# Performance work log

Measured on AMD Instinct MI355X. Metric: run time of the kernel, lower is better.

Reference implementation:

```python
import jax, jax.numpy as jnp
import numpy as np

N, E, G = 100000, 1600000, 5000
F_IN, H = 128, 3
C1, C2, C3 = 64, 32, 16
SLOPE = 0.2


def _gat_conv(x, W, a_src, a_dst, b, src, dst, n_nodes, heads, ch):
    # x: [N, F_in] -> h: [N, H, C]
    h = (x @ W).reshape(n_nodes, heads, ch)
    alpha_s = jnp.sum(h * a_src, axis=-1)  # [N, H]
    alpha_d = jnp.sum(h * a_dst, axis=-1)  # [N, H]
    e = jax.nn.leaky_relu(alpha_s[src] + alpha_d[dst], SLOPE)  # [E, H]
    # segment softmax over destination nodes (numerically stable)
    e_max = jax.ops.segment_max(e, dst, num_segments=n_nodes)
    e_max = jnp.where(jnp.isfinite(e_max), e_max, 0.0)
    ex = jnp.exp(e - e_max[dst])
    denom = jax.ops.segment_sum(ex, dst, num_segments=n_nodes)
    alpha = ex / (denom[dst] + 1e-16)  # [E, H]
    msg = h[src] * alpha[:, :, None]  # [E, H, C]
    out = jax.ops.segment_sum(msg, dst, num_segments=n_nodes)  # [N, H, C]
    return out.reshape(n_nodes, heads * ch) + b


def setup_inputs() -> dict:
    key = jax.random.key(0)
    ks = jax.random.split(key, 20)
    def w(k, shape, fan_in):
        return jax.random.normal(k, shape, jnp.float32) / np.sqrt(fan_in)
    return {
        "x": jax.random.normal(ks[0], (N, F_IN), jnp.float32),
        "y": jax.random.uniform(ks[1], (G,), jnp.float32),
        "edge_index": jax.random.randint(ks[2], (2, E), 0, N, jnp.int32),
        "batch": jnp.sort(jax.random.randint(ks[3], (N,), 0, G, jnp.int32)),
        "W1": w(ks[4], (F_IN, H * C1), F_IN),
        "as1": w(ks[5], (H, C1), C1),
        "ad1": w(ks[6], (H, C1), C1),
        "b1": jnp.zeros((H * C1,), jnp.float32),
        "W2": w(ks[7], (H * C1, H * C2), H * C1),
        "as2": w(ks[8], (H, C2), C2),
        "ad2": w(ks[9], (H, C2), C2),
        "b2": jnp.zeros((H * C2,), jnp.float32),
        "W3": w(ks[10], (H * C2, H * C3), H * C2),
        "as3": w(ks[11], (H, C3), C3),
        "ad3": w(ks[12], (H, C3), C3),
        "b3": jnp.zeros((H * C3,), jnp.float32),
        "Wl": w(ks[13], (H * C3, 1), H * C3),
        "bl": jnp.zeros((1,), jnp.float32),
    }


def reference(x, y, edge_index, batch, W1, as1, ad1, b1, W2, as2, ad2, b2,
              W3, as3, ad3, b3, Wl, bl):
    n = x.shape[0]
    loops = jnp.arange(n, dtype=edge_index.dtype)
    src = jnp.concatenate([edge_index[0], loops])  # PyG add_self_loops=True
    dst = jnp.concatenate([edge_index[1], loops])

    h = _gat_conv(x, W1, as1, ad1, b1, src, dst, n, H, C1)
    h = jax.nn.elu(h)
    h = _gat_conv(h, W2, as2, ad2, b2, src, dst, n, H, C2)
    h = jax.nn.elu(h)
    h = _gat_conv(h, W3, as3, ad3, b3, src, dst, n, H, C3)

    # global mean pool over graphs
    counts = jax.ops.segment_sum(jnp.ones((n,), h.dtype), batch, num_segments=G)
    pooled = jax.ops.segment_sum(h, batch, num_segments=G) / jnp.maximum(counts, 1.0)[:, None]
    pooled = jax.nn.relu(pooled)

    logits = pooled @ Wl + bl  # [G, 1]
    t = y.reshape(-1, 1)
    loss = jnp.mean(jax.nn.softplus(logits) - t * logits)  # BCEWithLogits
    out = jax.nn.sigmoid(logits)
    return out, loss
```

## Files before the change

### kernel.cpp

```cpp
#include <hip/hip_runtime.h>
#include <hip/hip_bf16.h>

#define THREADS 256
typedef __hip_bfloat16 bf16;

typedef __bf16 v8bf __attribute__((ext_vector_type(8)));
typedef float  v4f  __attribute__((ext_vector_type(4)));

__device__ __forceinline__ float bfl(unsigned u){ return __uint_as_float(u << 16); }
__device__ __forceinline__ float bfh(unsigned u){ return __uint_as_float(u & 0xffff0000u); }

__global__ void hist_k(const int* __restrict__ ei, int* __restrict__ cnt,
                       int* __restrict__ rank, int E, int ET){
  int i = blockIdx.x*THREADS + threadIdx.x;
  if (i >= ET) return;
  int d = (i < E) ? ei[E + i] : (i - E);
  rank[i] = atomicAdd(&cnt[d], 1);
}

__global__ void scan1_k(const int* __restrict__ deg, int* __restrict__ off,
                        int* __restrict__ bsum, int n){
  __shared__ int sh[1024];
  int i = blockIdx.x*1024 + threadIdx.x;
  int v = (i < n) ? deg[i] : 0;
  sh[threadIdx.x] = v;
  __syncthreads();
  for (int s = 1; s < 1024; s <<= 1){
    int t = (threadIdx.x >= s) ? sh[threadIdx.x - s] : 0;
    __syncthreads();
    sh[threadIdx.x] += t;
    __syncthreads();
  }
  if (i < n) off[i+1] = sh[threadIdx.x];
  if (threadIdx.x == 1023) bsum[blockIdx.x] = sh[1023];
}

__global__ void scan2_k(int* __restrict__ bsum, int nb){
  __shared__ int sh[256];
  int v = (threadIdx.x < nb) ? bsum[threadIdx.x] : 0;
  sh[threadIdx.x] = v;
  __syncthreads();
  for (int s = 1; s < 256; s <<= 1){
    int t = (threadIdx.x >= s) ? sh[threadIdx.x - s] : 0;
    __syncthreads();
    sh[threadIdx.x] += t;
    __syncthreads();
  }
  if (threadIdx.x < nb) bsum[threadIdx.x] = sh[threadIdx.x] - v;
}

__global__ void scan3_k(int* __restrict__ off, const int* __restrict__ bsum, int n){
  int i = blockIdx.x*1024 + threadIdx.x;
  if (i < n) off[i+1] += bsum[blockIdx.x];
  if (i == 0) off[0] = 0;
}

__global__ void scatter_k(const int* __restrict__ ei, const int* __restrict__ off,
                          const int* __restrict__ rank, int* __restrict__ csr,
                          int E, int ET){
  int i = blockIdx.x*THREADS + threadIdx.x;
  if (i >= ET) return;
  int s, d;
  if (i < E){ s = ei[i]; d = ei[E+i]; } else { s = i - E; d = i - E; }
  csr[off[d] + rank[i]] = s;
}

__global__ void convf2b_k(const float4* __restrict__ in, uint2* __restrict__ out, int n4){
  int i = blockIdx.x*THREADS + threadIdx.x;
  if (i >= n4) return;
  float4 v = in[i];
  union { bf16 h[4]; uint2 u; } cv;
  cv.h[0] = __float2bfloat16(v.x); cv.h[1] = __float2bfloat16(v.y);
  cv.h[2] = __float2bfloat16(v.z); cv.h[3] = __float2bfloat16(v.w);
  out[i] = cv.u;
}

__device__ __forceinline__ void wt_do(const float* __restrict__ W, bf16* __restrict__ WT,
                                      int K, int COUT, int i){
  int k = i / COUT, c = i - k*COUT;
  WT[(size_t)c*K + k] = __float2bfloat16(W[i]);
}

__device__ __forceinline__ void va_do(const float* __restrict__ W, const float* __restrict__ as,
                                      const float* __restrict__ ad, bf16* __restrict__ WTX,
                                      int K, int C, int COUT, int i){
  int k = i % K, c6 = i / K;
  int h = (c6 < 3) ? c6 : c6 - 3;
  const float* a = ((c6 < 3) ? as : ad) + h*C;
  const float* wp = W + (size_t)k*COUT + h*C;
  float s = 0.f;
  for (int cc = 0; cc < C; cc++) s += wp[cc]*a[cc];
  WTX[(size_t)(COUT + c6)*K + k] = __float2bfloat16(s);
}

__global__ void prep_k(const float* __restrict__ W1, const float* __restrict__ as1, const float* __restrict__ ad1,
                       const float* __restrict__ W2, const float* __restrict__ as2, const float* __restrict__ ad2,
                       const float* __restrict__ W3, const float* __restrict__ as3, const float* __restrict__ ad3,
                       bf16* __restrict__ WT1, bf16* __restrict__ WT2, bf16* __restrict__ WT3,
                       const int* __restrict__ batch, int* __restrict__ goff, int n, int G)
{
  int i = blockIdx.x*THREADS + threadIdx.x;
  if (i < 24576){ wt_do(W1, WT1, 128, 192, i); return; } i -= 24576;
  if (i < 18432){ wt_do(W2, WT2, 192, 96, i); return; }  i -= 18432;
  if (i < 4608) { wt_do(W3, WT3, 96, 48, i); return; }   i -= 4608;
  if (i < 768)  { va_do(W1, as1, ad1, WT1, 128, 64, 192, i); return; } i -= 768;
  if (i < 1152) { va_do(W2, as2, ad2, WT2, 192, 32, 96, i); return; }  i -= 1152;
  if (i < 576)  { va_do(W3, as3, ad3, WT3, 96, 16, 48, i); return; }   i -= 576;
  if (i <= G){
    if (i == G){ goff[G] = n; return; }
    int lo = 0, hi = n;
    while (lo < hi){ int mid = (lo + hi) >> 1; if (batch[mid] < i) lo = mid + 1; else hi = mid; }
    goff[i] = lo;
  }
}

template<int K, int COUT>
__global__ void __launch_bounds__(256) gemm_mfma_k(
    const bf16* __restrict__ A, const bf16* __restrict__ BT,
    bf16* __restrict__ C, float* __restrict__ aS4, float* __restrict__ aD4,
    int nRowTiles)
{
  int wave = threadIdx.x >> 6, lane = threadIdx.x & 63;
  int rt = blockIdx.x*4 + wave;
  if (rt >= nRowTiles) return;
  int half = lane & 15;
  int quad = lane >> 4;
  const __bf16* aBase = (const __bf16*)A + (size_t)(rt*16 + half)*K + quad*8;
  v8bf aF[K/32];
  #pragma unroll
  for (int kk = 0; kk < K/32; kk++) aF[kk] = *(const v8bf*)(aBase + kk*32);
  #pragma unroll
  for (int cb = 0; cb < COUT + 16; cb += 16){
    const __bf16* bBase = (const __bf16*)BT + (size_t)(cb + half)*K + quad*8;
    v4f acc = {0.f, 0.f, 0.f, 0.f};
    #pragma unroll
    for (int kk = 0; kk < K/32; kk++)
      acc = __builtin_amdgcn_mfma_f32_16x16x32_bf16(aF[kk], *(const v8bf*)(bBase + kk*32), acc, 0, 0, 0);
    int orow = rt*16 + quad*4;
    if (cb < COUT){
      bf16* cp = C + (size_t)orow*COUT + cb + half;
      #pragma unroll
      for (int r = 0; r < 4; r++)
        cp[(size_t)r*COUT] = __float2bfloat16(acc[r]);
    } else if (half < 6){
      #pragma unroll
      for (int r = 0; r < 4; r++){
        int row = orow + r;
        if (half < 3) aS4[row*4 + half]     = acc[r];
        else          aD4[row*4 + half - 3] = acc[r];
      }
    }
  }
}

template<int HC, int CSH, int GRP>
__global__ void __launch_bounds__(256) agg_k(
    const int* __restrict__ off, const int* __restrict__ csr,
    const bf16* __restrict__ hbuf,
    const float* __restrict__ aS4, const float* __restrict__ aD4,
    const float* __restrict__ bias,
    float* __restrict__ outF, bf16* __restrict__ outB,
    int n, int doElu)
{
  constexpr int NPW = 64 / GRP;
  __shared__ __align__(16) float wls[4][384];
  int tid = threadIdx.x;
  int wave = tid >> 6;
  int lane = tid & 63;
  int q = lane % GRP;
  int grp = lane / GRP;
  int wv = (blockIdx.x*256 + tid) >> 6;
  int node = wv*NPW + grp;
  bool valid = node < n;
  int e0 = 0, e1 = 0;
  float4 ad = {0.f, 0.f, 0.f, 0.f};
  if (valid){
    e0 = off[node]; e1 = off[node+1];
    ad = *(const float4*)(aD4 + 4*node);
  }
  const int hq = (4*q) >> CSH;
  const bool act = valid && (q < HC/4);
  const size_t hoff = 4*q;
  float dh = 0.f;
  float a0 = 0.f, a1 = 0.f, a2 = 0.f, a3 = 0.f;
  float* gbase = &wls[wave][grp*3*GRP*2];
  const float* wh = gbase + hq*GRP*2;

  int nch = (e1 - e0 + GRP - 1) / GRP;
  for (int c = 0; c < nch; c++){
    int base = e0 + c*GRP;
    __threadfence_block();
    int j = base + q;
    if (j < e1){
      int s = csr[j];
      float4 av = *(const float4*)(aS4 + 4*s);
      float x0 = av.x + ad.x; x0 = (x0 > 0.f) ? x0 : 0.2f*x0;
      float x1 = av.y + ad.y; x1 = (x1 > 0.f) ? x1 : 0.2f*x1;
      float x2 = av.z + ad.z; x2 = (x2 > 0.f) ? x2 : 0.2f*x2;
      float sf = __int_as_float(s);
      float2 p0 = {__expf(x0), sf};
      float2 p1 = {__expf(x1), sf};
      float2 p2 = {__expf(x2), sf};
      *(float2*)(gbase + (0*GRP + q)*2) = p0;
      *(float2*)(gbase + (1*GRP + q)*2) = p1;
      *(float2*)(gbase + (2*GRP + q)*2) = p2;
    }
    __threadfence_block();
    if (act){
      int lim = e1 - base; if (lim > GRP) lim = GRP;
      int jj = 0;
      for (; jj + 8 <= lim; jj += 8){
        float4 pA = *(const float4*)(wh + jj*2);
        float4 pB = *(const float4*)(wh + jj*2 + 4);
        float4 pC = *(const float4*)(wh + jj*2 + 8);
        float4 pD = *(const float4*)(wh + jj*2 + 12);
        int s0 = __float_as_int(pA.y), s1 = __float_as_int(pA.w);
        int s2 = __float_as_int(pB.y), s3 = __float_as_int(pB.w);
        int s4 = __float_as_int(pC.y), s5 = __float_as_int(pC.w);
        int s6 = __float_as_int(pD.y), s7 = __float_as_int(pD.w);
        float w0 = pA.x, w1 = pA.z, w2 = pB.x, w3 = pB.z;
        float w4 = pC.x, w5 = pC.z, w6 = pD.x, w7 = pD.z;
        uint2 u0 = *(const uint2*)(hbuf + (size_t)s0*HC + hoff);
        uint2 u1 = *(const uint2*)(hbuf + (size_t)s1*HC + hoff);
        uint2 u2 = *(const uint2*)(hbuf + (size_t)s2*HC + hoff);
        uint2 u3 = *(const uint2*)(hbuf + (size_t)s3*HC + hoff);
        uint2 u4 = *(const uint2*)(hbuf + (size_t)s4*HC + hoff);
        uint2 u5 = *(const uint2*)(hbuf + (size_t)s5*HC + hoff);
        uint2 u6 = *(const uint2*)(hbuf + (size_t)s6*HC + hoff);
        uint2 u7 = *(const uint2*)(hbuf + (size_t)s7*HC + hoff);
        dh += w0 + w1 + w2 + w3 + w4 + w5 + w6 + w7;
        a0 += w0*bfl(u0.x); a1 += w0*bfh(u0.x); a2 += w0*bfl(u0.y); a3 += w0*bfh(u0.y);
        a0 += w1*bfl(u1.x); a1 += w1*bfh(u1.x); a2 += w1*bfl(u1.y); a3 += w1*bfh(u1.y);
        a0 += w2*bfl(u2.x); a1 += w2*bfh(u2.x); a2 += w2*bfl(u2.y); a3 += w2*bfh(u2.y);
        a0 += w3*bfl(u3.x); a1 += w3*bfh(u3.x); a2 += w3*bfl(u3.y); a3 += w3*bfh(u3.y);
        a0 += w4*bfl(u4.x); a1 += w4*bfh(u4.x); a2 += w4*bfl(u4.y); a3 += w4*bfh(u4.y);
        a0 += w5*bfl(u5.x); a1 += w5*bfh(u5.x); a2 += w5*bfl(u5.y); a3 += w5*bfh(u5.y);
        a0 += w6*bfl(u6.x); a1 += w6*bfh(u6.x); a2 += w6*bfl(u6.y); a3 += w6*bfh(u6.y);
        a0 += w7*bfl(u7.x); a1 += w7*bfh(u7.x); a2 += w7*bfl(u7.y); a3 += w7*bfh(u7.y);
      }
      for (; jj + 4 <= lim; jj += 4){
        float4 pA = *(const float4*)(wh + jj*2);
        float4 pB = *(const float4*)(wh + jj*2 + 4);
        int s0 = __float_as_int(pA.y), s1 = __float_as_int(pA.w);
        int s2 = __float_as_int(pB.y), s3 = __float_as_int(pB.w);
        float w0 = pA.x, w1 = pA.z, w2 = pB.x, w3 = pB.z;
        uint2 u0 = *(const uint2*)(hbuf + (size_t)s0*HC + hoff);
        uint2 u1 = *(const uint2*)(hbuf + (size_t)s1*HC + hoff);
        uint2 u2 = *(const uint2*)(hbuf + (size_t)s2*HC + hoff);
        uint2 u3 = *(const uint2*)(hbuf + (size_t)s3*HC + hoff);
        dh += w0 + w1 + w2 + w3;
        a0 += w0*bfl(u0.x); a1 += w0*bfh(u0.x); a2 += w0*bfl(u0.y); a3 += w0*bfh(u0.y);
        a0 += w1*bfl(u1.x); a1 += w1*bfh(u1.x); a2 += w1*bfl(u1.y); a3 += w1*bfh(u1.y);
        a0 += w2*bfl(u2.x); a1 += w2*bfh(u2.x); a2 += w2*bfl(u2.y); a3 += w2*bfh(u2.y);
        a0 += w3*bfl(u3.x); a1 += w3*bfh(u3.x); a2 += w3*bfl(u3.y); a3 += w3*bfh(u3.y);
      }
      for (; jj < lim; jj++){
        float2 pw = *(const float2*)(wh + jj*2);
        int s = __float_as_int(pw.y);
        float w = pw.x;
        uint2 u = *(const uint2*)(hbuf + (size_t)s*HC + hoff);
        dh += w;
        a0 += w*bfl(u.x); a1 += w*bfh(u.x); a2 += w*bfl(u.y); a3 += w*bfh(u.y);
      }
    }
  }
  if (act){
    float inv = 1.f / (dh + 1e-16f);
    const float4 b = *(const float4*)(bias + 4*q);
    float r0 = a0*inv + b.x, r1 = a1*inv + b.y, r2 = a2*inv + b.z, r3 = a3*inv + b.w;
    if (doElu){
      r0 = (r0 > 0.f) ? r0 : (__expf(r0) - 1.f);
      r1 = (r1 > 0.f) ? r1 : (__expf(r1) - 1.f);
      r2 = (r2 > 0.f) ? r2 : (__expf(r2) - 1.f);
      r3 = (r3 > 0.f) ? r3 : (__expf(r3) - 1.f);
    }
    if (outF){
      float4 o = {r0, r1, r2, r3};
      *(float4*)(outF + (size_t)node*HC + 4*q) = o;
    }
    if (outB){
      union { bf16 h[4]; uint2 u; } cv;
      cv.h[0] = __float2bfloat16(r0); cv.h[1] = __float2bfloat16(r1);
      cv.h[2] = __float2bfloat16(r2); cv.h[3] = __float2bfloat16(r3);
      *(uint2*)(outB + (size_t)node*HC + 4*q) = cv.u;
    }
  }
}

__global__ void __launch_bounds__(256) pool_logits_k(
    const float* __restrict__ h3, const int* __restrict__ goff,
    const float* __restrict__ Wl, const float* __restrict__ bl,
    const float* __restrict__ y, float* __restrict__ outp,
    float* __restrict__ lossAcc, int G)
{
  int lane = threadIdx.x & 63;
  int g = (blockIdx.x*256 + threadIdx.x) >> 6;
  if (g >= G) return;
  int n0 = goff[g], n1 = goff[g+1];
  int cnt = n1 - n0;
  float acc = 0.f, acc2 = 0.f, wl = 0.f;
  if (lane < 48){
    wl = Wl[lane];
    const float* p = h3 + (size_t)n0*48 + lane;
    int i = 0;
    for (; i + 2 <= cnt; i += 2){ acc += p[(size_t)i*48]; acc2 += p[(size_t)(i+1)*48]; }
    if (i < cnt) acc += p[(size_t)i*48];
    acc += acc2;
  }
  float inv = 1.f / fmaxf((float)cnt, 1.f);
  float v = fmaxf(acc*inv, 0.f) * wl;
  for (int o = 32; o > 0; o >>= 1) v += __shfl_down(v, o);
  if (lane == 0){
    float logit = v + bl[0];
    outp[g] = 1.f / (1.f + __expf(-logit));
    float t = y[g];
    float sp = (logit > 0.f) ? (logit + log1pf(__expf(-logit))) : log1pf(__expf(logit));
    atomicAdd(lossAcc, sp - t*logit);
  }
}

__global__ void fin_k(const float* __restrict__ lossAcc, float* __restrict__ outp, int gtot){
  outp[gtot] = lossAcc[0] / (float)gtot;
}

extern "C" void kernel_launch(void* const* d_in, const int* in_sizes, int n_in,
                              void* d_out, int out_size, void* d_ws, size_t ws_size,
                              hipStream_t stream)
{
  (void)n_in; (void)out_size; (void)ws_size;
  const float* x    = (const float*)d_in[0];
  const float* y    = (const float*)d_in[1];
  const int*  ei    = (const int*)d_in[2];
  const int*  batch = (const int*)d_in[3];
  const float* W1 = (const float*)d_in[4];
  const float* as1= (const float*)d_in[5];
  const float* ad1= (const float*)d_in[6];
  const float* b1 = (const float*)d_in[7];
  const float* W2 = (const float*)d_in[8];
  const float* as2= (const float*)d_in[9];
  const float* ad2= (const float*)d_in[10];
  const float* b2 = (const float*)d_in[11];
  const float* W3 = (const float*)d_in[12];
  const float* as3= (const float*)d_in[13];
  const float* ad3= (const float*)d_in[14];
  const float* b3 = (const float*)d_in[15];
  const float* Wl = (const float*)d_in[16];
  const float* bl = (const float*)d_in[17];
  float* outp = (float*)d_out;

  int Nn = in_sizes[0] / 128;
  int Gg = in_sizes[1];
  int Ee = in_sizes[2] / 2;
  int ET = Ee + Nn;

  char* p = (char*)d_ws;
  auto carve = [&](size_t bytes) -> void* {
    void* r = (void*)p; p += (bytes + 255) & ~(size_t)255; return r;
  };
  int*   off     = (int*)  carve((size_t)(Nn+1)*4);
  int*   cnt     = (int*)  carve((size_t)Nn*4);
  int*   csr     = (int*)  carve((size_t)ET*4);
  int*   rank    = (int*)  carve((size_t)ET*4);
  int*   bsum    = (int*)  carve(256*4);
  float* aS4     = (float*)carve((size_t)Nn*4*4);
  float* aD4     = (float*)carve((size_t)Nn*4*4);
  int*   goff    = (int*)  carve((size_t)(Gg+1)*4);
  float* lossAcc = (float*)carve(4);
  bf16*  WT1     = (bf16*) carve((size_t)(192+16)*128*2);
  bf16*  WT2     = (bf16*) carve((size_t)(96+16)*192*2);
  bf16*  WT3     = (bf16*) carve((size_t)(48+16)*96*2);
  bf16*  bufH    = (bf16*) carve((size_t)Nn*192*2);
  bf16*  bufA    = (bf16*) carve((size_t)Nn*192*2);
  float* bufO    = (float*)((char*)bufH + ((size_t)Nn*96 + 255 & ~(size_t)255));

  int NB = (Nn + 1023) / 1024;
  int ebk = (ET + THREADS - 1) / THREADS;

  hipMemsetAsync(cnt, 0, (size_t)Nn*4, stream);
  hist_k<<<ebk, THREADS, 0, stream>>>(ei, cnt, rank, Ee, ET);
  scan1_k<<<NB, 1024, 0, stream>>>(cnt, off, bsum, Nn);
  scan2_k<<<1, 256, 0, stream>>>(bsum, NB);
  scan3_k<<<NB, 1024, 0, stream>>>(off, bsum, Nn);
  scatter_k<<<ebk, THREADS, 0, stream>>>(ei, off, rank, csr, Ee, ET);

  convf2b_k<<<(Nn*32 + THREADS-1)/THREADS, THREADS, 0, stream>>>((const float4*)x, (uint2*)bufA, Nn*32);
  int prepTot = 24576 + 18432 + 4608 + 768 + 1152 + 576 + (Gg + 1);
  prep_k<<<(prepTot + THREADS-1)/THREADS, THREADS, 0, stream>>>(
      W1, as1, ad1, W2, as2, ad2, W3, as3, ad3, WT1, WT2, WT3, batch, goff, Nn, Gg);

  int nRT = Nn / 16;
  int gx  = (nRT + 3) / 4;
  int gb1 = (Nn + 3) / 4;
  int gb2 = (Nn + 7) / 8;
  int gb3 = (Nn + 15) / 16;

  gemm_mfma_k<128,192><<<gx, 256, 0, stream>>>(bufA, WT1, bufH, aS4, aD4, nRT);
  agg_k<192,6,64><<<gb1, 256, 0, stream>>>(off, csr, bufH, aS4, aD4, b1, nullptr, bufA, Nn, 1);
  gemm_mfma_k<192,96><<<gx, 256, 0, stream>>>(bufA, WT2, bufH, aS4, aD4, nRT);
  agg_k<96,5,32><<<gb2, 256, 0, stream>>>(off, csr, bufH, aS4, aD4, b2, nullptr, bufA, Nn, 1);
  gemm_mfma_k<96,48><<<gx, 256, 0, stream>>>(bufA, WT3, bufH, aS4, aD4, nRT);
  agg_k<48,4,16><<<gb3, 256, 0, stream>>>(off, csr, bufH, aS4, aD4, b3, bufO, nullptr, Nn, 0);

  hipMemsetAsync(lossAcc, 0, 4, stream);
  pool_logits_k<<<(Gg + 3)/4, 256, 0, stream>>>(bufO, goff, Wl, bl, y, outp, lossAcc, Gg);
  fin_k<<<1, 1, 0, stream>>>(lossAcc, outp, Gg);
}
```

Baseline: 629.5 us.

## Fuse fp32-to-bf16 input conversion into first GEMM; persistent-grid aggregation with byte offsets

New measurement: 655.2 us. +4.1%, slower.

```diff
diff --git a/kernel.cpp b/kernel.cpp
--- a/kernel.cpp
+++ b/kernel.cpp
@@ -6,6 +6,7 @@
 
 typedef __bf16 v8bf __attribute__((ext_vector_type(8)));
 typedef float  v4f  __attribute__((ext_vector_type(4)));
+typedef unsigned int v2u __attribute__((ext_vector_type(2)));
 
 __device__ __forceinline__ float bfl(unsigned u){ return __uint_as_float(u << 16); }
 __device__ __forceinline__ float bfh(unsigned u){ return __uint_as_float(u & 0xffff0000u); }
@@ -63,16 +64,6 @@
   int s, d;
   if (i < E){ s = ei[i]; d = ei[E+i]; } else { s = i - E; d = i - E; }
   csr[off[d] + rank[i]] = s;
-}
-
-__global__ void convf2b_k(const float4* __restrict__ in, uint2* __restrict__ out, int n4){
-  int i = blockIdx.x*THREADS + threadIdx.x;
-  if (i >= n4) return;
-  float4 v = in[i];
-  union { bf16 h[4]; uint2 u; } cv;
-  cv.h[0] = __float2bfloat16(v.x); cv.h[1] = __float2bfloat16(v.y);
-  cv.h[2] = __float2bfloat16(v.z); cv.h[3] = __float2bfloat16(v.w);
-  out[i] = cv.u;
 }
 
 __device__ __forceinline__ void wt_do(const float* __restrict__ W, bf16* __restrict__ WT,
@@ -114,9 +105,9 @@
   }
 }
 
-template<int K, int COUT>
+template<int K, int COUT, bool CVT>
 __global__ void __launch_bounds__(256) gemm_mfma_k(
-    const bf16* __restrict__ A, const bf16* __restrict__ BT,
+    const void* __restrict__ Av, const bf16* __restrict__ BT,
     bf16* __restrict__ C, float* __restrict__ aS4, float* __restrict__ aD4,
     int nRowTiles)
 {
@@ -125,10 +116,23 @@
   if (rt >= nRowTiles) return;
   int half = lane & 15;
   int quad = lane >> 4;
-  const __bf16* aBase = (const __bf16*)A + (size_t)(rt*16 + half)*K + quad*8;
   v8bf aF[K/32];
-  #pragma unroll
-  for (int kk = 0; kk < K/32; kk++) aF[kk] = *(const v8bf*)(aBase + kk*32);
+  if constexpr (CVT){
+    const float* aBase = (const float*)Av + (size_t)(rt*16 + half)*K + quad*8;
+    #pragma unroll
+    for (int kk = 0; kk < K/32; kk++){
+      float4 f0 = *(const float4*)(aBase + kk*32);
+      float4 f1 = *(const float4*)(aBase + kk*32 + 4);
+      v8bf t;
+      t[0] = (__bf16)f0.x; t[1] = (__bf16)f0.y; t[2] = (__bf16)f0.z; t[3] = (__bf16)f0.w;
+      t[4] = (__bf16)f1.x; t[5] = (__bf16)f1.y; t[6] = (__bf16)f1.z; t[7] = (__bf16)f1.w;
+      aF[kk] = t;
+    }
+  } else {
+    const __bf16* aBase = (const __bf16*)Av + (size_t)(rt*16 + half)*K + quad*8;
+    #pragma unroll
+    for (int kk = 0; kk < K/32; kk++) aF[kk] = *(const v8bf*)(aBase + kk*32);
+  }
   #pragma unroll
   for (int cb = 0; cb < COUT + 16; cb += 16){
     const __bf16* bBase = (const __bf16*)BT + (size_t)(cb + half)*K + quad*8;
@@ -169,120 +173,126 @@
   int lane = tid & 63;
   int q = lane % GRP;
   int grp = lane / GRP;
-  int wv = (blockIdx.x*256 + tid) >> 6;
-  int node = wv*NPW + grp;
-  bool valid = node < n;
-  int e0 = 0, e1 = 0;
-  float4 ad = {0.f, 0.f, 0.f, 0.f};
-  if (valid){
-    e0 = off[node]; e1 = off[node+1];
-    ad = *(const float4*)(aD4 + 4*node);
-  }
   const int hq = (4*q) >> CSH;
-  const bool act = valid && (q < HC/4);
-  const size_t hoff = 4*q;
-  float dh = 0.f;
-  float a0 = 0.f, a1 = 0.f, a2 = 0.f, a3 = 0.f;
+  const bool act = q < HC/4;
+  const unsigned q8 = 8u*q;
   float* gbase = &wls[wave][grp*3*GRP*2];
   const float* wh = gbase + hq*GRP*2;
-
-  int nch = (e1 - e0 + GRP - 1) / GRP;
-  for (int c = 0; c < nch; c++){
-    int base = e0 + c*GRP;
-    __threadfence_block();
-    int j = base + q;
-    if (j < e1){
-      int s = csr[j];
-      float4 av = *(const float4*)(aS4 + 4*s);
-      float x0 = av.x + ad.x; x0 = (x0 > 0.f) ? x0 : 0.2f*x0;
-      float x1 = av.y + ad.y; x1 = (x1 > 0.f) ? x1 : 0.2f*x1;
-      float x2 = av.z + ad.z; x2 = (x2 > 0.f) ? x2 : 0.2f*x2;
-      float sf = __int_as_float(s);
-      float2 p0 = {__expf(x0), sf};
-      float2 p1 = {__expf(x1), sf};
-      float2 p2 = {__expf(x2), sf};
-      *(float2*)(gbase + (0*GRP + q)*2) = p0;
-      *(float2*)(gbase + (1*GRP + q)*2) = p1;
-      *(float2*)(gbase + (2*GRP + q)*2) = p2;
+  const char* hb = (const char*)hbuf;
+  float4 bv = {0.f, 0.f, 0.f, 0.f};
+  if (act) bv = *(const float4*)(bias + 4*q);
+
+  int nodeTot = (n + NPW - 1) / NPW;
+  int nwv = gridDim.x * 4;
+  for (int wv = (blockIdx.x*256 + tid) >> 6; wv < nodeTot; wv += nwv){
+    int node = wv*NPW + grp;
+    bool valid = node < n;
+    int e0 = 0, e1 = 0;
+    float4 ad = {0.f, 0.f, 0.f, 0.f};
+    if (valid){
+      e0 = off[node]; e1 = off[node+1];
+      ad = *(const float4*)(aD4 + 4*node);
     }
-    __threadfence_block();
-    if (act){
-      int lim = e1 - base; if (lim > GRP) lim = GRP;
-      int jj = 0;
-      for (; jj + 8 <= lim; jj += 8){
-        float4 pA = *(const float4*)(wh + jj*2);
-        float4 pB = *(const float4*)(wh + jj*2 + 4);
-        float4 pC = *(const float4*)(wh + jj*2 + 8);
-        float4 pD = *(const float4*)(wh + jj*2 + 12);
-        int s0 = __float_as_int(pA.y), s1 = __float_as_int(pA.w);
-        int s2 = __float_as_int(pB.y), s3 = __float_as_int(pB.w);
-        int s4 = __float_as_int(pC.y), s5 = __float_as_int(pC.w);
-        int s6 = __float_as_int(pD.y), s7 = __float_as_int(pD.w);
-        float w0 = pA.x, w1 = pA.z, w2 = pB.x, w3 = pB.z;
-        float w4 = pC.x, w5 = pC.z, w6 = pD.x, w7 = pD.z;
-        uint2 u0 = *(const uint2*)(hbuf + (size_t)s0*HC + hoff);
-        uint2 u1 = *(const uint2*)(hbuf + (size_t)s1*HC + hoff);
-        uint2 u2 = *(const uint2*)(hbuf + (size_t)s2*HC + hoff);
-        uint2 u3 = *(const uint2*)(hbuf + (size_t)s3*HC + hoff);
-        uint2 u4 = *(const uint2*)(hbuf + (size_t)s4*HC + hoff);
-        uint2 u5 = *(const uint2*)(hbuf + (size_t)s5*HC + hoff);
-        uint2 u6 = *(const uint2*)(hbuf + (size_t)s6*HC + hoff);
-        uint2 u7 = *(const uint2*)(hbuf + (size_t)s7*HC + hoff);
-        dh += w0 + w1 + w2 + w3 + w4 + w5 + w6 + w7;
-        a0 += w0*bfl(u0.x); a1 += w0*bfh(u0.x); a2 += w0*bfl(u0.y); a3 += w0*bfh(u0.y);
-        a0 += w1*bfl(u1.x); a1 += w1*bfh(u1.x); a2 += w1*bfl(u1.y); a3 += w1*bfh(u1.y);
-        a0 += w2*bfl(u2.x); a1 += w2*bfh(u2.x); a2 += w2*bfl(u2.y); a3 += w2*bfh(u2.y);
-        a0 += w3*bfl(u3.x); a1 += w3*bfh(u3.x); a2 += w3*bfl(u3.y); a3 += w3*bfh(u3.y);
-        a0 += w4*bfl(u4.x); a1 += w4*bfh(u4.x); a2 += w4*bfl(u4.y); a3 += w4*bfh(u4.y);
-        a0 += w5*bfl(u5.x); a1 += w5*bfh(u5.x); a2 += w5*bfl(u5.y); a3 += w5*bfh(u5.y);
-        a0 += w6*bfl(u6.x); a1 += w6*bfh(u6.x); a2 += w6*bfl(u6.y); a3 += w6*bfh(u6.y);
-        a0 += w7*bfl(u7.x); a1 += w7*bfh(u7.x); a2 += w7*bfl(u7.y); a3 += w7*bfh(u7.y);
-      }
-      for (; jj + 4 <= lim; jj += 4){
-        float4 pA = *(const float4*)(wh + jj*2);
-        float4 pB = *(const float4*)(wh + jj*2 + 4);
-        int s0 = __float_as_int(pA.y), s1 = __float_as_int(pA.w);
-        int s2 = __float_as_int(pB.y), s3 = __float_as_int(pB.w);
-        float w0 = pA.x, w1 = pA.z, w2 = pB.x, w3 = pB.z;
-        uint2 u0 = *(const uint2*)(hbuf + (size_t)s0*HC + hoff);
-        uint2 u1 = *(const uint2*)(hbuf + (size_t)s1*HC + hoff);
-        uint2 u2 = *(const uint2*)(hbuf + (size_t)s2*HC + hoff);
-        uint2 u3 = *(const uint2*)(hbuf + (size_t)s3*HC + hoff);
-        dh += w0 + w1 + w2 + w3;
-        a0 += w0*bfl(u0.x); a1 += w0*bfh(u0.x); a2 += w0*bfl(u0.y); a3 += w0*bfh(u0.y);
-        a0 += w1*bfl(u1.x); a1 += w1*bfh(u1.x); a2 += w1*bfl(u1.y); a3 += w1*bfh(u1.y);
-        a0 += w2*bfl(u2.x); a1 += w2*bfh(u2.x); a2 += w2*bfl(u2.y); a3 += w2*bfh(u2.y);
-        a0 += w3*bfl(u3.x); a1 += w3*bfh(u3.x); a2 += w3*bfl(u3.y); a3 += w3*bfh(u3.y);
-      }
-      for (; jj < lim; jj++){
-        float2 pw = *(const float2*)(wh + jj*2);
-        int s = __float_as_int(pw.y);
-        float w = pw.x;
-        uint2 u = *(const uint2*)(hbuf + (size_t)s*HC + hoff);
-        dh += w;
-        a0 += w*bfl(u.x); a1 += w*bfh(u.x); a2 += w*bfl(u.y); a3 += w*bfh(u.y);
+    float dh = 0.f;
+    float a0 = 0.f, a1 = 0.f, a2 = 0.f, a3 = 0.f;
+
+    int nch = (e1 - e0 + GRP - 1) / GRP;
+    for (int c = 0; c < nch; c++){
+      int base = e0 + c*GRP;
+      __threadfence_block();
+      int j = base + q;
+      if (j < e1){
+        int s = __builtin_nontemporal_load(&csr[j]);
+        float4 av = *(const float4*)(aS4 + 4*s);
+        float x0 = av.x + ad.x; x0 = (x0 > 0.f) ? x0 : 0.2f*x0;
+        float x1 = av.y + ad.y; x1 = (x1 > 0.f) ? x1 : 0.2f*x1;
+        float x2 = av.z + ad.z; x2 = (x2 > 0.f) ? x2 : 0.2f*x2;
+        float sf = __int_as_float(s * (HC*2));
+        float2 p0 = {__expf(x0), sf};
+        float2 p1 = {__expf(x1), sf};
+        float2 p2 = {__expf(x2), sf};
+        *(float2*)(gbase + (0*GRP + q)*2) = p0;
+        *(float2*)(gbase + (1*GRP + q)*2) = p1;
+        *(float2*)(gbase + (2*GRP + q)*2) = p2;
+      }
+      __threadfence_block();
+      if (act){
+        int lim = e1 - base; if (lim > GRP) lim = GRP;
+        int jj = 0;
+        for (; jj + 8 <= lim; jj += 8){
+          float4 pA = *(const float4*)(wh + jj*2);
+          float4 pB = *(const float4*)(wh + jj*2 + 4);
+          float4 pC = *(const float4*)(wh + jj*2 + 8);
+          float4 pD = *(const float4*)(wh + jj*2 + 12);
+          unsigned o0 = __float_as_uint(pA.y) + q8, o1 = __float_as_uint(pA.w) + q8;
+          unsigned o2 = __float_as_uint(pB.y) + q8, o3 = __float_as_uint(pB.w) + q8;
+          unsigned o4 = __float_as_uint(pC.y) + q8, o5 = __float_as_uint(pC.w) + q8;
+          unsigned o6 = __float_as_uint(pD.y) + q8, o7 = __float_as_uint(pD.w) + q8;
+          float w0 = pA.x, w1 = pA.z, w2 = pB.x, w3 = pB.z;
+          float w4 = pC.x, w5 = pC.z, w6 = pD.x, w7 = pD.z;
+          uint2 u0 = *(const uint2*)(hb + o0);
+          uint2 u1 = *(const uint2*)(hb + o1);
+          uint2 u2 = *(const uint2*)(hb + o2);
+          uint2 u3 = *(const uint2*)(hb + o3);
+          uint2 u4 = *(const uint2*)(hb + o4);
+          uint2 u5 = *(const uint2*)(hb + o5);
+          uint2 u6 = *(const uint2*)(hb + o6);
+          uint2 u7 = *(const uint2*)(hb + o7);
+          dh += w0 + w1 + w2 + w3 + w4 + w5 + w6 + w7;
+          a0 += w0*bfl(u0.x); a1 += w0*bfh(u0.x); a2 += w0*bfl(u0.y); a3 += w0*bfh(u0.y);
+          a0 += w1*bfl(u1.x); a1 += w1*bfh(u1.x); a2 += w1*bfl(u1.y); a3 += w1*bfh(u1.y);
+          a0 += w2*bfl(u2.x); a1 += w2*bfh(u2.x); a2 += w2*bfl(u2.y); a3 += w2*bfh(u2.y);
+          a0 += w3*bfl(u3.x); a1 += w3*bfh(u3.x); a2 += w3*bfl(u3.y); a3 += w3*bfh(u3.y);
+          a0 += w4*bfl(u4.x); a1 += w4*bfh(u4.x); a2 += w4*bfl(u4.y); a3 += w4*bfh(u4.y);
+          a0 += w5*bfl(u5.x); a1 += w5*bfh(u5.x); a2 += w5*bfl(u5.y); a3 += w5*bfh(u5.y);
+          a0 += w6*bfl(u6.x); a1 += w6*bfh(u6.x); a2 += w6*bfl(u6.y); a3 += w6*bfh(u6.y);
+          a0 += w7*bfl(u7.x); a1 += w7*bfh(u7.x); a2 += w7*bfl(u7.y); a3 += w7*bfh(u7.y);
+        }
+        for (; jj + 4 <= lim; jj += 4){
+          float4 pA = *(const float4*)(wh + jj*2);
+          float4 pB = *(const float4*)(wh + jj*2 + 4);
+          unsigned o0 = __float_as_uint(pA.y) + q8, o1 = __float_as_uint(pA.w) + q8;
+          unsigned o2 = __float_as_uint(pB.y) + q8, o3 = __float_as_uint(pB.w) + q8;
+          float w0 = pA.x, w1 = pA.z, w2 = pB.x, w3 = pB.z;
+          uint2 u0 = *(const uint2*)(hb + o0);
+          uint2 u1 = *(const uint2*)(hb + o1);
+          uint2 u2 = *(const uint2*)(hb + o2);
+          uint2 u3 = *(const uint2*)(hb + o3);
+          dh += w0 + w1 + w2 + w3;
+          a0 += w0*bfl(u0.x); a1 += w0*bfh(u0.x); a2 += w0*bfl(u0.y); a3 += w0*bfh(u0.y);
+          a0 += w1*bfl(u1.x); a1 += w1*bfh(u1.x); a2 += w1*bfl(u1.y); a3 += w1*bfh(u1.y);
+          a0 += w2*bfl(u2.x); a1 += w2*bfh(u2.x); a2 += w2*bfl(u2.y); a3 += w2*bfh(u2.y);
+          a0 += w3*bfl(u3.x); a1 += w3*bfh(u3.x); a2 += w3*bfl(u3.y); a3 += w3*bfh(u3.y);
+        }
+        for (; jj < lim; jj++){
+          float2 pw = *(const float2*)(wh + jj*2);
+          unsigned o = __float_as_uint(pw.y) + q8;
+          float w = pw.x;
+          uint2 u = *(const uint2*)(hb + o);
+          dh += w;
+          a0 += w*bfl(u.x); a1 += w*bfh(u.x); a2 += w*bfl(u.y); a3 += w*bfh(u.y);
+        }
       }
     }
-  }
-  if (act){
-    float inv = 1.f / (dh + 1e-16f);
-    const float4 b = *(const float4*)(bias + 4*q);
-    float r0 = a0*inv + b.x, r1 = a1*inv + b.y, r2 = a2*inv + b.z, r3 = a3*inv + b.w;
-    if (doElu){
-      r0 = (r0 > 0.f) ? r0 : (__expf(r0) - 1.f);
-      r1 = (r1 > 0.f) ? r1 : (__expf(r1) - 1.f);
-      r2 = (r2 > 0.f) ? r2 : (__expf(r2) - 1.f);
-      r3 = (r3 > 0.f) ? r3 : (__expf(r3) - 1.f);
-    }
-    if (outF){
-      float4 o = {r0, r1, r2, r3};
-      *(float4*)(outF + (size_t)node*HC + 4*q) = o;
-    }
-    if (outB){
-      union { bf16 h[4]; uint2 u; } cv;
-      cv.h[0] = __float2bfloat16(r0); cv.h[1] = __float2bfloat16(r1);
-      cv.h[2] = __float2bfloat16(r2); cv.h[3] = __float2bfloat16(r3);
-      *(uint2*)(outB + (size_t)node*HC + 4*q) = cv.u;
+    if (act && valid){
+      float inv = 1.f / (dh + 1e-16f);
+      float r0 = a0*inv + bv.x, r1 = a1*inv + bv.y, r2 = a2*inv + bv.z, r3 = a3*inv + bv.w;
+      if (doElu){
+        r0 = (r0 > 0.f) ? r0 : (__expf(r0) - 1.f);
+        r1 = (r1 > 0.f) ? r1 : (__expf(r1) - 1.f);
+        r2 = (r2 > 0.f) ? r2 : (__expf(r2) - 1.f);
+        r3 = (r3 > 0.f) ? r3 : (__expf(r3) - 1.f);
+      }
+      if (outF){
+        v4f o = {r0, r1, r2, r3};
+        __builtin_nontemporal_store(o, (v4f*)(outF + (size_t)node*HC + 4*q));
+      }
+      if (outB){
+        union { bf16 h[4]; v2u u; } cv;
+        cv.h[0] = __float2bfloat16(r0); cv.h[1] = __float2bfloat16(r1);
+        cv.h[2] = __float2bfloat16(r2); cv.h[3] = __float2bfloat16(r3);
+        __builtin_nontemporal_store(cv.u, (v2u*)(outB + (size_t)node*HC + 4*q));
+      }
     }
   }
 }
@@ -383,23 +393,20 @@
   scan3_k<<<NB, 1024, 0, stream>>>(off, bsum, Nn);
   scatter_k<<<ebk, THREADS, 0, stream>>>(ei, off, rank, csr, Ee, ET);
 
-  convf2b_k<<<(Nn*32 + THREADS-1)/THREADS, THREADS, 0, stream>>>((const float4*)x, (uint2*)bufA, Nn*32);
   int prepTot = 24576 + 18432 + 4608 + 768 + 1152 + 576 + (Gg + 1);
   prep_k<<<(prepTot + THREADS-1)/THREADS, THREADS, 0, stream>>>(
       W1, as1, ad1, W2, as2, ad2, W3, as3, ad3, WT1, WT2, WT3, batch, goff, Nn, Gg);
 
   int nRT = Nn / 16;
   int gx  = (nRT + 3) / 4;
-  int gb1 = (Nn + 3) / 4;
-  int gb2 = (Nn + 7) / 8;
-  int gb3 = (Nn + 15) / 16;
-
-  gemm_mfma_k<128,192><<<gx, 256, 0, stream>>>(bufA, WT1, bufH, aS4, aD4, nRT);
-  agg_k<192,6,64><<<gb1, 256, 0, stream>>>(off, csr, bufH, aS4, aD4, b1, nullptr, bufA, Nn, 1);
-  gemm_mfma_k<192,96><<<gx, 256, 0, stream>>>(bufA, WT2, bufH, aS4, aD4, nRT);
-  agg_k<96,5,32><<<gb2, 256, 0, stream>>>(off, csr, bufH, aS4, aD4, b2, nullptr, bufA, Nn, 1);
-  gemm_mfma_k<96,48><<<gx, 256, 0, stream>>>(bufA, WT3, bufH, aS4, aD4, nRT);
-  agg_k<48,4,16><<<gb3, 256, 0, stream>>>(off, csr, bufH, aS4, aD4, b3, bufO, nullptr, Nn, 0);
+  int aggGrid = 2048;
+
+  gemm_mfma_k<128,192,true><<<gx, 256, 0, stream>>>(x, WT1, bufH, aS4, aD4, nRT);
+  agg_k<192,6,64><<<aggGrid, 256, 0, stream>>>(off, csr, bufH, aS4, aD4, b1, nullptr, bufA, Nn, 1);
+  gemm_mfma_k<192,96,false><<<gx, 256, 0, stream>>>(bufA, WT2, bufH, aS4, aD4, nRT);
+  agg_k<96,5,32><<<aggGrid, 256, 0, stream>>>(off, csr, bufH, aS4, aD4, b2, nullptr, bufA, Nn, 1);
+  gemm_mfma_k<96,48,false><<<gx, 256, 0, stream>>>(bufA, WT3, bufH, aS4, aD4, nRT);
+  agg_k<48,4,16><<<aggGrid, 256, 0, stream>>>(off, csr, bufH, aS4, aD4, b3, bufO, nullptr, Nn, 0);
 
   hipMemsetAsync(lossAcc, 0, 4, stream);
   pool_logits_k<<<(Gg + 3)/4, 256, 0, stream>>>(bufO, goff, Wl, bl, y, outp, lossAcc, Gg);
```
